# Performance work log

Hardware: AMD Instinct MI355X
Metric: run time of the kernel (lower is better)

Reference implementation:

```python
import jax, jax.numpy as jnp
import numpy as np

B, T, F, U = 64, 2048, 256, 32


def setup_inputs() -> dict:
    key = jax.random.key(0)
    k0, k1, k2, k3, k4 = jax.random.split(key, 5)
    return {
        "x": jax.random.normal(k0, (B, T, F), jnp.float32),
        "kernel": jax.random.normal(k1, (F, U), jnp.float32) * (1.0 / np.sqrt(F)),
        "bias": jnp.zeros((U,), jnp.float32),
        "chain_kernel": jax.random.normal(k2, (U, U), jnp.float32) * 0.1,
        "left_boundary": jax.random.normal(k3, (U,), jnp.float32) * 0.1,
        "right_boundary": jax.random.normal(k4, (U,), jnp.float32) * 0.1,
    }


def _potentials(x, kernel, bias, left_boundary, right_boundary):
    # Dense (linear activation) + boundary energies at first/last timestep (mask=None path)
    pot = jnp.einsum("btf,fu->btu", x, kernel) + bias
    pot = pot.at[:, 0, :].add(left_boundary)
    pot = pot.at[:, -1, :].add(right_boundary)
    return pot  # [B, T, U]


def _viterbi(pot, chain):
    # pot: [B,T,U], chain: [U,U]; max-plus forward recursion + backtrack
    init = pot[:, 0]  # [B,U]

    def fwd(state, pot_t):
        # scores[b,i,j] = state[b,i] + chain[i,j]
        scores = state[:, :, None] + chain[None]
        bp = jnp.argmax(scores, axis=1).astype(jnp.int32)  # [B,U] backpointers
        new_state = jnp.max(scores, axis=1) + pot_t        # [B,U]
        return new_state, bp

    last, bps = jax.lax.scan(fwd, init, jnp.swapaxes(pot, 0, 1)[1:])  # bps: [T-1,B,U]
    best_score = jnp.max(last, axis=-1)                   # [B]
    last_tag = jnp.argmax(last, axis=-1).astype(jnp.int32)  # [B]

    def back(tag, bp_t):
        prev = jnp.take_along_axis(bp_t, tag[:, None], axis=1)[:, 0]
        return prev, prev

    _, tags_rev = jax.lax.scan(back, last_tag, bps[::-1])  # [T-1,B]
    tags = jnp.concatenate([tags_rev[::-1], last_tag[None]], axis=0)  # [T,B]
    return jnp.swapaxes(tags, 0, 1).astype(jnp.int32), best_score


def reference(x, kernel, bias, chain_kernel, left_boundary, right_boundary):
    pot = _potentials(x, kernel, bias, left_boundary, right_boundary)
    decoded, _ = _viterbi(pot, chain_kernel)
    return decoded  # [B, T] int32
```

## Files before the change

### kernel.cpp

```cpp
#include <hip/hip_runtime.h>
#include <hip/hip_bf16.h>
#include <cstdint>

#define BB 64
#define TT 2048
#define FD 256
#define UU 32

__global__ __launch_bounds__(64) void potentials_kernel(
    const float* __restrict__ x, const float* __restrict__ K,
    const float* __restrict__ bias, const float* __restrict__ lb,
    const float* __restrict__ rb, float* __restrict__ pot)
{
    __shared__ __align__(16) float lds[16384];
    float* xs = lds;
    float* Kt = lds + 8192;

    const int tid = threadIdx.x;
    const int ug = tid & 7;
    const int rg = tid >> 3;

    for (int j = 0; j < 128; ++j) {
        const int e = j * 64 + tid;
        const int f = e >> 5;
        const int u = e & 31;
        Kt[u * 256 + (((f >> 2) ^ (u & 7)) << 2) + (f & 3)] = K[e];
    }

    float bu[4], lu4[4], ru4[4];
    #pragma unroll
    for (int m = 0; m < 4; ++m) {
        bu[m]  = bias[ug + 8 * m];
        lu4[m] = lb[ug + 8 * m];
        ru4[m] = rb[ug + 8 * m];
    }

    const int tiles = (BB * TT) / 32;
    for (int tile = blockIdx.x; tile < tiles; tile += gridDim.x) {
        const int row0 = tile * 32;
        __syncthreads();
        #pragma unroll 4
        for (int k = 0; k < 32; ++k) {
            const float4 v = *(const float4*)(x + (size_t)(row0 + k) * FD + tid * 4);
            *(float4*)&xs[k * 256 + ((tid ^ (k & 7)) << 2)] = v;
        }
        __syncthreads();

        float acc[4][4];
        #pragma unroll
        for (int i = 0; i < 4; ++i)
            #pragma unroll
            for (int m = 0; m < 4; ++m) acc[i][m] = 0.f;

        #pragma unroll 4
        for (int q = 0; q < 64; ++q) {
            float4 xq[4], kq[4];
            #pragma unroll
            for (int i = 0; i < 4; ++i)
                xq[i] = *(const float4*)&xs[(rg + 8 * i) * 256 + ((q ^ rg) << 2)];
            #pragma unroll
            for (int m = 0; m < 4; ++m)
                kq[m] = *(const float4*)&Kt[(ug + 8 * m) * 256 + ((q ^ ug) << 2)];
            #pragma unroll
            for (int i = 0; i < 4; ++i)
                #pragma unroll
                for (int m = 0; m < 4; ++m) {
                    acc[i][m] += xq[i].x * kq[m].x;
                    acc[i][m] += xq[i].y * kq[m].y;
                    acc[i][m] += xq[i].z * kq[m].z;
                    acc[i][m] += xq[i].w * kq[m].w;
                }
        }

        #pragma unroll
        for (int i = 0; i < 4; ++i) {
            const int row = row0 + rg + 8 * i;
            const int t = row & (TT - 1);
            #pragma unroll
            for (int m = 0; m < 4; ++m) {
                pot[(size_t)row * UU + ug + 8 * m] =
                    acc[i][m] + bu[m] + (t == 0 ? lu4[m] : 0.f)
                              + (t == TT - 1 ? ru4[m] : 0.f);
            }
        }
    }
}

__device__ __forceinline__ float quad_swap(float v) {
    const int i = __float_as_int(v);
    const int r = __builtin_amdgcn_update_dpp(i, i, 0xB1, 0xF, 0xF, true);
    return __int_as_float(r);
}

__global__ __launch_bounds__(64) void vit_values_kernel(
    const float* __restrict__ pot, const float* __restrict__ chain,
    float* __restrict__ chk)
{
    __shared__ __align__(16) float mbuf[32];

    const int lane = threadIdx.x;
    const int u = lane >> 1;
    const int q = lane & 1;
    const int qb = 16 * q;
    const int b = blockIdx.x;
    const float* pb = pot + (size_t)b * TT * UU;

    float cc[16];
    #pragma unroll
    for (int i = 0; i < 16; ++i) cc[i] = chain[(qb + i) * UU + u];

    float s[16];
    {
        const float4* s0 = (const float4*)(pb + qb);
        #pragma unroll
        for (int k = 0; k < 4; ++k) {
            const float4 v = s0[k];
            s[4*k+0] = v.x; s[4*k+1] = v.y; s[4*k+2] = v.z; s[4*k+3] = v.w;
        }
    }

    auto step = [&](float potv, int t) {
        float a[16];
        #pragma unroll
        for (int i = 0; i < 16; ++i) a[i] = s[i] + cc[i];
        float m8[8];
        #pragma unroll
        for (int i = 0; i < 8; ++i) m8[i] = fmaxf(a[2*i], a[2*i+1]);
        float m4[4];
        #pragma unroll
        for (int i = 0; i < 4; ++i) m4[i] = fmaxf(m8[2*i], m8[2*i+1]);
        const float pm = fmaxf(fmaxf(m4[0], m4[1]), fmaxf(m4[2], m4[3]));
        const float om = quad_swap(pm);
        const float mm = fmaxf(pm, om) + potv;

        mbuf[u] = mm;

        if ((t & 63) == 63)
            chk[((size_t)b * 33 + ((t >> 6) + 1)) * UU + u] = mm;

        const float4 x0 = *(const float4*)&mbuf[qb + 0];
        const float4 x1 = *(const float4*)&mbuf[qb + 4];
        const float4 x2 = *(const float4*)&mbuf[qb + 8];
        const float4 x3 = *(const float4*)&mbuf[qb + 12];
        s[0]=x0.x;  s[1]=x0.y;  s[2]=x0.z;  s[3]=x0.w;
        s[4]=x1.x;  s[5]=x1.y;  s[6]=x1.z;  s[7]=x1.w;
        s[8]=x2.x;  s[9]=x2.y;  s[10]=x2.z; s[11]=x2.w;
        s[12]=x3.x; s[13]=x3.y; s[14]=x3.z; s[15]=x3.w;
    };

    float pr[8], pn[8];
    #pragma unroll
    for (int j = 0; j < 8; ++j) pr[j] = pb[(1 + j) * UU + u];

    #pragma unroll 1
    for (int g = 0; g < 255; ++g) {
        #pragma unroll
        for (int j = 0; j < 8; ++j) {
            int tp = 9 + 8 * g + j;
            if (tp > TT - 1) tp = TT - 1;
            pn[j] = pb[tp * UU + u];
        }
        const int t0 = 1 + 8 * g;
        #pragma unroll
        for (int j = 0; j < 8; ++j)
            step(pr[j], t0 + j);
        #pragma unroll
        for (int j = 0; j < 8; ++j) pr[j] = pn[j];
    }
    #pragma unroll
    for (int j = 0; j < 7; ++j)
        step(pr[j], 2041 + j);
}

__global__ __launch_bounds__(64) void vit_window_kernel(
    const float* __restrict__ pot, const float* __restrict__ chain,
    const float* __restrict__ chk, unsigned char* __restrict__ Mg,
    unsigned char* __restrict__ bpg)
{
    __shared__ float potL[64 * 32];
    __shared__ float mbuf[32];

    const int lane = threadIdx.x;
    const int u = lane & 31;
    const int h = lane >> 5;
    const int hbase = 16 * h;
    const int w = blockIdx.x;
    const int b = blockIdx.y;
    const float* pb = pot + (size_t)b * TT * UU;
    const int r0 = 64 * w;

    {
        const float4* src = (const float4*)(pb + (size_t)r0 * UU);
        float4* dst = (float4*)potL;
        #pragma unroll
        for (int k = 0; k < 8; ++k) dst[lane + 64 * k] = src[lane + 64 * k];
    }
    __syncthreads();

    float cc[16];
    #pragma unroll
    for (int i = 0; i < 16; ++i) cc[i] = chain[(hbase + i) * UU + u];

    float s[16];
    if (w == 0) {
        #pragma unroll
        for (int i = 0; i < 16; ++i) s[i] = potL[hbase + i];
    } else {
        #pragma unroll
        for (int i = 0; i < 16; ++i) s[i] = chk[((size_t)b * 33 + w) * UU + hbase + i];
    }

    int orig = u;
    unsigned char* bb = bpg + (size_t)b * (TT - 1) * UU;

    const int tl0 = (w == 0) ? 1 : 0;
    #pragma unroll 1
    for (int tl = tl0; tl < 64; ++tl) {
        const int t = r0 + tl;
        const float potv = potL[tl * UU + u];

        float a[16];
        #pragma unroll
        for (int i = 0; i < 16; ++i) a[i] = s[i] + cc[i];

        float v8[8]; int i8[8];
        #pragma unroll
        for (int i = 0; i < 8; ++i) {
            const bool c = a[2*i+1] > a[2*i];
            v8[i] = c ? a[2*i+1] : a[2*i];
            i8[i] = c ? (2*i+1) : (2*i);
        }
        float v4[4]; int i4[4];
        #pragma unroll
        for (int i = 0; i < 4; ++i) {
            const bool c = v8[2*i+1] > v8[2*i];
            v4[i] = c ? v8[2*i+1] : v8[2*i];
            i4[i] = c ? i8[2*i+1] : i8[2*i];
        }
        float v2[2]; int i2[2];
        #pragma unroll
        for (int i = 0; i < 2; ++i) {
            const bool c = v4[2*i+1] > v4[2*i];
            v2[i] = c ? v4[2*i+1] : v4[2*i];
            i2[i] = c ? i4[2*i+1] : i4[2*i];
        }
        const bool cf = v2[1] > v2[0];
        const float pv = cf ? v2[1] : v2[0];
        const int pidx = hbase + (cf ? i2[1] : i2[0]);

        const float opv = __shfl_xor(pv, 32, 64);
        const int   opi = __shfl_xor(pidx, 32, 64);
        const bool take = h ? (opv >= pv) : (opv > pv);
        const int  mv   = take ? opi : pidx;
        const float mm  = fmaxf(pv, opv) + potv;

        if (h == 0) bb[(size_t)(t - 1) * UU + u] = (unsigned char)mv;
        orig = __shfl(orig, mv, 64);

        mbuf[u] = mm;
        const float4 x0 = *(const float4*)&mbuf[hbase + 0];
        const float4 x1 = *(const float4*)&mbuf[hbase + 4];
        const float4 x2 = *(const float4*)&mbuf[hbase + 8];
        const float4 x3 = *(const float4*)&mbuf[hbase + 12];
        s[0]=x0.x; s[1]=x0.y; s[2]=x0.z;  s[3]=x0.w;
        s[4]=x1.x; s[5]=x1.y; s[6]=x1.z;  s[7]=x1.w;
        s[8]=x2.x; s[9]=x2.y; s[10]=x2.z; s[11]=x2.w;
        s[12]=x3.x; s[13]=x3.y; s[14]=x3.z; s[15]=x3.w;
    }

    if (h == 0) Mg[(size_t)b * 1024 + w * UU + u] = (unsigned char)orig;
}

__global__ __launch_bounds__(64) void vit_backtrack_kernel(
    const float* __restrict__ chk, const unsigned char* __restrict__ Mg,
    const unsigned char* __restrict__ bpg, int* __restrict__ out)
{
    __shared__ __align__(16) unsigned char bp[(TT - 1) * UU];

    const int lane = threadIdx.x;
    const int b = blockIdx.x;
    const unsigned char* bb = bpg + (size_t)b * (TT - 1) * UU;

    #pragma unroll 4
    for (int i = 0; i < 64; ++i) {
        const int idx = i * 64 + lane;
        if (idx < 4094)
            ((int4*)bp)[idx] = ((const int4*)bb)[idx];
    }

    float fv = (lane < 32) ? chk[((size_t)b * 33 + 32) * UU + lane] : -INFINITY;
    int fi = lane & 31;
    #pragma unroll
    for (int mask = 16; mask >= 1; mask >>= 1) {
        const float ov = __shfl_xor(fv, mask, 64);
        const int oi = __shfl_xor(fi, mask, 64);
        if (ov > fv || (ov == fv && oi < fi)) { fv = ov; fi = oi; }
    }
    int bt = __shfl(fi, 0, 64);

    int my_btag = 0;
    #pragma unroll 1
    for (int w = 31; w >= 0; --w) {
        if (lane == w) my_btag = bt;
        bt = Mg[(size_t)b * 1024 + w * 32 + bt];
    }

    __syncthreads();

    if (lane < 32) {
        const int w = lane;
        int tag = my_btag;
        int t = w * 64 + 63;
        int* ob = out + (size_t)b * TT;
        ob[t] = tag;
        #pragma unroll 1
        for (; t >= w * 64 + 1; --t) {
            tag = bp[(t - 1) * UU + tag];
            ob[t - 1] = tag;
        }
    }
}

extern "C" void kernel_launch(void* const* d_in, const int* in_sizes, int n_in,
                              void* d_out, int out_size, void* d_ws, size_t ws_size,
                              hipStream_t stream)
{
    const float* x     = (const float*)d_in[0];
    const float* K     = (const float*)d_in[1];
    const float* bias  = (const float*)d_in[2];
    const float* chain = (const float*)d_in[3];
    const float* lb    = (const float*)d_in[4];
    const float* rb    = (const float*)d_in[5];
    int* out = (int*)d_out;

    float* pot = (float*)d_ws;
    float* chk = pot + (size_t)BB * TT * UU;
    unsigned char* Mg  = (unsigned char*)(chk + (size_t)BB * 33 * UU);
    unsigned char* bpg = Mg + (size_t)BB * 32 * UU;

    potentials_kernel<<<512, 64, 0, stream>>>(x, K, bias, lb, rb, pot);
    vit_values_kernel<<<BB, 64, 0, stream>>>(pot, chain, chk);
    vit_window_kernel<<<dim3(32, BB), 64, 0, stream>>>(pot, chain, chk, Mg, bpg);
    vit_backtrack_kernel<<<BB, 64, 0, stream>>>(chk, Mg, bpg, out);
}
```

Baseline: 529.7 us.

## Replace LDS state exchange in Viterbi forward pass with cross-lane permute butterfly

Result: no change. 537.3 us (+1.4%).

```diff
diff --git a/kernel.cpp b/kernel.cpp
--- a/kernel.cpp
+++ b/kernel.cpp
@@ -6,6 +6,15 @@
 #define TT 2048
 #define FD 256
 #define UU 32
+
+#if defined(__has_builtin)
+#  if __has_builtin(__builtin_amdgcn_permlane16_swap) && __has_builtin(__builtin_amdgcn_permlane32_swap)
+#    define HAVE_PLSWAP 1
+#  endif
+#endif
+#ifndef HAVE_PLSWAP
+#  define HAVE_PLSWAP 0
+#endif
 
 __global__ __launch_bounds__(64) void potentials_kernel(
     const float* __restrict__ x, const float* __restrict__ K,
@@ -86,90 +95,166 @@
     }
 }
 
-__device__ __forceinline__ float quad_swap(float v) {
-    const int i = __float_as_int(v);
-    const int r = __builtin_amdgcn_update_dpp(i, i, 0xB1, 0xF, 0xF, true);
-    return __int_as_float(r);
-}
+template<int CTRL>
+__device__ __forceinline__ float dppf(float v) {
+    return __int_as_float(__builtin_amdgcn_update_dpp(
+        __float_as_int(v), __float_as_int(v), CTRL, 0xF, 0xF, true));
+}
+
+__device__ __forceinline__ float pl32max(float v) {
+#if HAVE_PLSWAP
+    auto r = __builtin_amdgcn_permlane32_swap(__float_as_uint(v), __float_as_uint(v),
+                                              false, false);
+    return fmaxf(__uint_as_float(r[0]), __uint_as_float(r[1]));
+#else
+    return fmaxf(v, __shfl_xor(v, 32, 64));
+#endif
+}
+
+__device__ __forceinline__ float pl16x(float v, bool xA) {
+#if HAVE_PLSWAP
+    auto r = __builtin_amdgcn_permlane16_swap(__float_as_uint(v), __float_as_uint(v),
+                                              false, false);
+    return xA ? __uint_as_float(r[0]) : __uint_as_float(r[1]);
+#else
+    (void)xA; return __shfl_xor(v, 16, 64);
+#endif
+}
+
+template<bool B> struct BoolC { static constexpr bool v = B; };
 
 __global__ __launch_bounds__(64) void vit_values_kernel(
     const float* __restrict__ pot, const float* __restrict__ chain,
     float* __restrict__ chk)
 {
-    __shared__ __align__(16) float mbuf[32];
+    __shared__ float mbuf[32];
 
     const int lane = threadIdx.x;
-    const int u = lane >> 1;
-    const int q = lane & 1;
-    const int qb = 16 * q;
+    const int u = lane & 31;
+    const int h = lane >> 5;
+    const int p = lane & 15;
     const int b = blockIdx.x;
     const float* pb = pot + (size_t)b * TT * UU;
 
-    float cc[16];
+    const bool own = (((lane >> 4) & 1) == h);
+
+    auto butterfly = [&](float V, float (&d)[16]) {
+        d[0]  = V;
+        d[1]  = dppf<0xB1>(V);
+        d[2]  = dppf<0x4E>(V);
+        d[3]  = dppf<0x1B>(V);
+        d[7]  = dppf<0x141>(V);
+        d[6]  = dppf<0x141>(d[1]);
+        d[5]  = dppf<0x141>(d[2]);
+        d[4]  = dppf<0x141>(d[3]);
+        d[15] = dppf<0x140>(V);
+        d[14] = dppf<0x140>(d[1]);
+        d[13] = dppf<0x140>(d[2]);
+        d[12] = dppf<0x140>(d[3]);
+        d[11] = dppf<0x140>(d[4]);
+        d[10] = dppf<0x140>(d[5]);
+        d[9]  = dppf<0x140>(d[6]);
+        d[8]  = dppf<0x140>(d[7]);
+    };
+
+    bool xA = false, ok16, ok32, bfok;
+#if HAVE_PLSWAP
+    {
+        auto r = __builtin_amdgcn_permlane16_swap((unsigned)lane, (unsigned)lane,
+                                                  false, false);
+        xA = ((int)r[0] == (lane ^ 16));
+        const bool xB = ((int)r[1] == (lane ^ 16));
+        ok16 = (__all((xA || xB) ? 1 : 0) != 0);
+    }
+    {
+        const bool e1 = (pl32max((float)lane)  == (float)(lane | 32));
+        const bool e2 = (pl32max(-(float)lane) == -(float)(lane & 31));
+        ok32 = (__all((e1 && e2) ? 1 : 0) != 0);
+    }
+#else
+    ok16 = true; ok32 = true;
+#endif
+    {
+        float W = (float)(p * 5 + 7);
+        float tb[16];
+        butterfly(W, tb);
+        bool ok = true;
+        #pragma unroll
+        for (int m = 0; m < 16; ++m)
+            ok = ok && (tb[m] == (float)((p ^ m) * 5 + 7));
+        bfok = (__all(ok ? 1 : 0) != 0);
+    }
+    const bool fastok = ok16 && ok32 && bfok;
+
+    float cc[16], s[16];
     #pragma unroll
-    for (int i = 0; i < 16; ++i) cc[i] = chain[(qb + i) * UU + u];
-
-    float s[16];
-    {
-        const float4* s0 = (const float4*)(pb + qb);
-        #pragma unroll
-        for (int k = 0; k < 4; ++k) {
-            const float4 v = s0[k];
-            s[4*k+0] = v.x; s[4*k+1] = v.y; s[4*k+2] = v.z; s[4*k+3] = v.w;
-        }
-    }
-
-    auto step = [&](float potv, int t) {
-        float a[16];
-        #pragma unroll
-        for (int i = 0; i < 16; ++i) a[i] = s[i] + cc[i];
-        float m8[8];
-        #pragma unroll
-        for (int i = 0; i < 8; ++i) m8[i] = fmaxf(a[2*i], a[2*i+1]);
-        float m4[4];
-        #pragma unroll
-        for (int i = 0; i < 4; ++i) m4[i] = fmaxf(m8[2*i], m8[2*i+1]);
-        const float pm = fmaxf(fmaxf(m4[0], m4[1]), fmaxf(m4[2], m4[3]));
-        const float om = quad_swap(pm);
-        const float mm = fmaxf(pm, om) + potv;
-
-        mbuf[u] = mm;
-
-        if ((t & 63) == 63)
-            chk[((size_t)b * 33 + ((t >> 6) + 1)) * UU + u] = mm;
-
-        const float4 x0 = *(const float4*)&mbuf[qb + 0];
-        const float4 x1 = *(const float4*)&mbuf[qb + 4];
-        const float4 x2 = *(const float4*)&mbuf[qb + 8];
-        const float4 x3 = *(const float4*)&mbuf[qb + 12];
-        s[0]=x0.x;  s[1]=x0.y;  s[2]=x0.z;  s[3]=x0.w;
-        s[4]=x1.x;  s[5]=x1.y;  s[6]=x1.z;  s[7]=x1.w;
-        s[8]=x2.x;  s[9]=x2.y;  s[10]=x2.z; s[11]=x2.w;
-        s[12]=x3.x; s[13]=x3.y; s[14]=x3.z; s[15]=x3.w;
+    for (int m = 0; m < 16; ++m) {
+        const int k = 16 * h + (p ^ m);
+        cc[m] = chain[k * UU + u];
+        s[m]  = pb[k];
+    }
+
+    auto run = [&](auto FC) {
+        constexpr bool FAST = decltype(FC)::v;
+
+        auto step = [&](float potv, int t) {
+            float a[16];
+            #pragma unroll
+            for (int m = 0; m < 16; ++m) a[m] = s[m] + cc[m];
+            const float r0 = fmaxf(fmaxf(a[0],  a[1]),  a[2]);
+            const float r1 = fmaxf(fmaxf(a[3],  a[4]),  a[5]);
+            const float r2 = fmaxf(fmaxf(a[6],  a[7]),  a[8]);
+            const float r3 = fmaxf(fmaxf(a[9],  a[10]), a[11]);
+            const float r4 = fmaxf(fmaxf(a[12], a[13]), a[14]);
+            const float r5 = fmaxf(fmaxf(r0, r1), r2);
+            const float r6 = fmaxf(fmaxf(r3, r4), a[15]);
+            const float pm = fmaxf(r5, r6);
+
+            float mx;
+            if constexpr (FAST) mx = pl32max(pm);
+            else                mx = fmaxf(pm, __shfl_xor(pm, 32, 64));
+            const float mm = mx + potv;
+
+            if (h == 0 && (t & 63) == 63)
+                chk[((size_t)b * 33 + ((t >> 6) + 1)) * UU + u] = mm;
+
+            if constexpr (FAST) {
+                const float X = pl16x(mm, xA);
+                const float V = own ? mm : X;
+                butterfly(V, s);
+            } else {
+                mbuf[u] = mm;
+                #pragma unroll
+                for (int m = 0; m < 16; ++m) s[m] = mbuf[16 * h + (p ^ m)];
+            }
+        };
+
+        float pr[8], pn[8];
+        #pragma unroll
+        for (int j = 0; j < 8; ++j) pr[j] = pb[(1 + j) * UU + u];
+
+        #pragma unroll 1
+        for (int g = 0; g < 255; ++g) {
+            #pragma unroll
+            for (int j = 0; j < 8; ++j) {
+                int tp = 9 + 8 * g + j;
+                if (tp > TT - 1) tp = TT - 1;
+                pn[j] = pb[tp * UU + u];
+            }
+            const int t0 = 1 + 8 * g;
+            #pragma unroll
+            for (int j = 0; j < 8; ++j)
+                step(pr[j], t0 + j);
+            #pragma unroll
+            for (int j = 0; j < 8; ++j) pr[j] = pn[j];
+        }
+        #pragma unroll
+        for (int j = 0; j < 7; ++j)
+            step(pr[j], 2041 + j);
     };
 
-    float pr[8], pn[8];
-    #pragma unroll
-    for (int j = 0; j < 8; ++j) pr[j] = pb[(1 + j) * UU + u];
-
-    #pragma unroll 1
-    for (int g = 0; g < 255; ++g) {
-        #pragma unroll
-        for (int j = 0; j < 8; ++j) {
-            int tp = 9 + 8 * g + j;
-            if (tp > TT - 1) tp = TT - 1;
-            pn[j] = pb[tp * UU + u];
-        }
-        const int t0 = 1 + 8 * g;
-        #pragma unroll
-        for (int j = 0; j < 8; ++j)
-            step(pr[j], t0 + j);
-        #pragma unroll
-        for (int j = 0; j < 8; ++j) pr[j] = pn[j];
-    }
-    #pragma unroll
-    for (int j = 0; j < 7; ++j)
-        step(pr[j], 2041 + j);
+    if (fastok) run(BoolC<true>{});
+    else        run(BoolC<false>{});
 }
 
 __global__ __launch_bounds__(64) void vit_window_kernel(
```

## Interleave four batch sequences per wavefront in Viterbi forward value pass

Applied to the files above, without the earlier changes.

Result: slower. 1.003 ms (+89.4%).

```diff
diff --git a/kernel.cpp b/kernel.cpp
--- a/kernel.cpp
+++ b/kernel.cpp
@@ -6,6 +6,7 @@
 #define TT 2048
 #define FD 256
 #define UU 32
+#define NC 4
 
 __global__ __launch_bounds__(64) void potentials_kernel(
     const float* __restrict__ x, const float* __restrict__ K,
@@ -96,33 +97,43 @@
     const float* __restrict__ pot, const float* __restrict__ chain,
     float* __restrict__ chk)
 {
-    __shared__ __align__(16) float mbuf[32];
+    __shared__ __align__(16) float mb[NC][32];
 
     const int lane = threadIdx.x;
     const int u = lane >> 1;
     const int q = lane & 1;
     const int qb = 16 * q;
-    const int b = blockIdx.x;
-    const float* pb = pot + (size_t)b * TT * UU;
+    const int b0 = blockIdx.x * NC;
+
+    const float* pb0 = pot + (size_t)(b0 + 0) * TT * UU;
+    const float* pb1 = pot + (size_t)(b0 + 1) * TT * UU;
+    const float* pb2 = pot + (size_t)(b0 + 2) * TT * UU;
+    const float* pb3 = pot + (size_t)(b0 + 3) * TT * UU;
 
     float cc[16];
     #pragma unroll
     for (int i = 0; i < 16; ++i) cc[i] = chain[(qb + i) * UU + u];
 
-    float s[16];
+    float s0[16], s1[16], s2[16], s3[16];
     {
-        const float4* s0 = (const float4*)(pb + qb);
+        const float4* a0 = (const float4*)(pb0 + qb);
+        const float4* a1 = (const float4*)(pb1 + qb);
+        const float4* a2 = (const float4*)(pb2 + qb);
+        const float4* a3 = (const float4*)(pb3 + qb);
         #pragma unroll
         for (int k = 0; k < 4; ++k) {
-            const float4 v = s0[k];
-            s[4*k+0] = v.x; s[4*k+1] = v.y; s[4*k+2] = v.z; s[4*k+3] = v.w;
-        }
-    }
-
-    auto step = [&](float potv, int t) {
+            const float4 v0 = a0[k], v1 = a1[k], v2 = a2[k], v3 = a3[k];
+            s0[4*k+0]=v0.x; s0[4*k+1]=v0.y; s0[4*k+2]=v0.z; s0[4*k+3]=v0.w;
+            s1[4*k+0]=v1.x; s1[4*k+1]=v1.y; s1[4*k+2]=v1.z; s1[4*k+3]=v1.w;
+            s2[4*k+0]=v2.x; s2[4*k+1]=v2.y; s2[4*k+2]=v2.z; s2[4*k+3]=v2.w;
+            s3[4*k+0]=v3.x; s3[4*k+1]=v3.y; s3[4*k+2]=v3.z; s3[4*k+3]=v3.w;
+        }
+    }
+
+    auto step = [&](float (&sc)[16], float* mbc, float potv, int t, int bb) {
         float a[16];
         #pragma unroll
-        for (int i = 0; i < 16; ++i) a[i] = s[i] + cc[i];
+        for (int i = 0; i < 16; ++i) a[i] = sc[i] + cc[i];
         float m8[8];
         #pragma unroll
         for (int i = 0; i < 8; ++i) m8[i] = fmaxf(a[2*i], a[2*i+1]);
@@ -133,43 +144,62 @@
         const float om = quad_swap(pm);
         const float mm = fmaxf(pm, om) + potv;
 
-        mbuf[u] = mm;
-
         if ((t & 63) == 63)
-            chk[((size_t)b * 33 + ((t >> 6) + 1)) * UU + u] = mm;
-
-        const float4 x0 = *(const float4*)&mbuf[qb + 0];
-        const float4 x1 = *(const float4*)&mbuf[qb + 4];
-        const float4 x2 = *(const float4*)&mbuf[qb + 8];
-        const float4 x3 = *(const float4*)&mbuf[qb + 12];
-        s[0]=x0.x;  s[1]=x0.y;  s[2]=x0.z;  s[3]=x0.w;
-        s[4]=x1.x;  s[5]=x1.y;  s[6]=x1.z;  s[7]=x1.w;
-        s[8]=x2.x;  s[9]=x2.y;  s[10]=x2.z; s[11]=x2.w;
-        s[12]=x3.x; s[13]=x3.y; s[14]=x3.z; s[15]=x3.w;
+            chk[((size_t)bb * 33 + ((t >> 6) + 1)) * UU + u] = mm;
+
+        mbc[u] = mm;
+        const float4 x0 = *(const float4*)&mbc[qb + 0];
+        const float4 x1 = *(const float4*)&mbc[qb + 4];
+        const float4 x2 = *(const float4*)&mbc[qb + 8];
+        const float4 x3 = *(const float4*)&mbc[qb + 12];
+        sc[0]=x0.x;  sc[1]=x0.y;  sc[2]=x0.z;  sc[3]=x0.w;
+        sc[4]=x1.x;  sc[5]=x1.y;  sc[6]=x1.z;  sc[7]=x1.w;
+        sc[8]=x2.x;  sc[9]=x2.y;  sc[10]=x2.z; sc[11]=x2.w;
+        sc[12]=x3.x; sc[13]=x3.y; sc[14]=x3.z; sc[15]=x3.w;
     };
 
-    float pr[8], pn[8];
-    #pragma unroll
-    for (int j = 0; j < 8; ++j) pr[j] = pb[(1 + j) * UU + u];
+    float pr0[4], pr1[4], pr2[4], pr3[4];
+    float pn0[4], pn1[4], pn2[4], pn3[4];
+    #pragma unroll
+    for (int j = 0; j < 4; ++j) {
+        pr0[j] = pb0[(1 + j) * UU + u];
+        pr1[j] = pb1[(1 + j) * UU + u];
+        pr2[j] = pb2[(1 + j) * UU + u];
+        pr3[j] = pb3[(1 + j) * UU + u];
+    }
 
     #pragma unroll 1
-    for (int g = 0; g < 255; ++g) {
-        #pragma unroll
-        for (int j = 0; j < 8; ++j) {
-            int tp = 9 + 8 * g + j;
+    for (int g = 0; g < 511; ++g) {
+        const int t0 = 1 + 4 * g;
+        #pragma unroll
+        for (int j = 0; j < 4; ++j) {
+            int tp = t0 + 4 + j;
             if (tp > TT - 1) tp = TT - 1;
-            pn[j] = pb[tp * UU + u];
-        }
-        const int t0 = 1 + 8 * g;
-        #pragma unroll
-        for (int j = 0; j < 8; ++j)
-            step(pr[j], t0 + j);
-        #pragma unroll
-        for (int j = 0; j < 8; ++j) pr[j] = pn[j];
-    }
-    #pragma unroll
-    for (int j = 0; j < 7; ++j)
-        step(pr[j], 2041 + j);
+            pn0[j] = pb0[tp * UU + u];
+            pn1[j] = pb1[tp * UU + u];
+            pn2[j] = pb2[tp * UU + u];
+            pn3[j] = pb3[tp * UU + u];
+        }
+        #pragma unroll
+        for (int j = 0; j < 4; ++j) {
+            step(s0, &mb[0][0], pr0[j], t0 + j, b0 + 0);
+            step(s1, &mb[1][0], pr1[j], t0 + j, b0 + 1);
+            step(s2, &mb[2][0], pr2[j], t0 + j, b0 + 2);
+            step(s3, &mb[3][0], pr3[j], t0 + j, b0 + 3);
+        }
+        #pragma unroll
+        for (int j = 0; j < 4; ++j) {
+            pr0[j] = pn0[j]; pr1[j] = pn1[j];
+            pr2[j] = pn2[j]; pr3[j] = pn3[j];
+        }
+    }
+    #pragma unroll
+    for (int j = 0; j < 3; ++j) {
+        step(s0, &mb[0][0], pr0[j], 2045 + j, b0 + 0);
+        step(s1, &mb[1][0], pr1[j], 2045 + j, b0 + 1);
+        step(s2, &mb[2][0], pr2[j], 2045 + j, b0 + 2);
+        step(s3, &mb[3][0], pr3[j], 2045 + j, b0 + 3);
+    }
 }
 
 __global__ __launch_bounds__(64) void vit_window_kernel(
@@ -339,7 +369,7 @@
     unsigned char* bpg = Mg + (size_t)BB * 32 * UU;
 
     potentials_kernel<<<512, 64, 0, stream>>>(x, K, bias, lb, rb, pot);
-    vit_values_kernel<<<BB, 64, 0, stream>>>(pot, chain, chk);
+    vit_values_kernel<<<BB / NC, 64, 0, stream>>>(pot, chain, chk);
     vit_window_kernel<<<dim3(32, BB), 64, 0, stream>>>(pot, chain, chk, Mg, bpg);
     vit_backtrack_kernel<<<BB, 64, 0, stream>>>(chk, Mg, bpg, out);
 }
```
